# Kernel tuning notes

Measured on AMD Instinct MI355X. Metric: run time of the kernel, lower is better.

Reference implementation:

```python
import jax, jax.numpy as jnp
import numpy as np


def _segment_sparsemax(x, batch, B):
    """Per-group sparsemax over a flat ragged tensor.

    x: [N] float values; batch: [N] sorted int group ids in [0, B).
    Groups are contiguous, so an in-group descending sort is a stable
    lexsort on (batch, -x); per-group cumsum is a global cumsum minus the
    cumsum value just before each group's start offset.
    """
    N = x.shape[0]
    num_nodes = jax.ops.segment_sum(jnp.ones(N, jnp.int32), batch, num_segments=B)  # [B]
    start = jnp.concatenate([jnp.zeros(1, jnp.int32), jnp.cumsum(num_nodes)[:-1]])  # [B]

    # shift by per-group max for numerical stability (as in torch forward)
    gmax = jax.ops.segment_max(x, batch, num_segments=B)
    xs = x - gmax[batch]

    # descending sort within each contiguous group
    order = jnp.lexsort((-xs, batch))
    sx = xs[order]  # [N], group-wise descending; group layout unchanged

    # per-group cumulative sum via global cumsum + start offsets
    cs = jnp.cumsum(sx)
    off = jnp.where(start > 0, cs[jnp.maximum(start - 1, 0)], jnp.zeros((), sx.dtype))  # [B]
    seg_cs = cs - off[batch] - 1.0  # input_cumsum - 1.0

    # rho = 1..n_g within each group
    rho = (jnp.arange(N, dtype=jnp.int32) - start[batch] + 1).astype(xs.dtype)

    support = rho * sx > seg_cs  # [N] bool
    supp_size = jax.ops.segment_sum(support.astype(jnp.int32), batch, num_segments=B)  # [B]

    idx = jnp.maximum(supp_size + start - 1, 0)  # [B]
    tau = seg_cs[idx] / supp_size.astype(xs.dtype)  # [B]

    return jnp.maximum(xs - tau[batch], 0.0)


def setup_inputs() -> dict:
    key = jax.random.key(0)
    k1, k2 = jax.random.split(key)
    N = 8_388_608
    B = 4096
    x = jax.random.normal(k1, (N,), dtype=jnp.float32)
    batch = jnp.sort(jax.random.randint(k2, (N,), 0, B)).astype(jnp.int64)
    return {"x": x, "batch": batch, "num_groups": B}


def reference(x, batch, num_groups):
    batch = batch.astype(jnp.int32)
    return _segment_sparsemax(x, batch, int(num_groups))
```

## Files before the change

kernel.cpp:

```cpp
#include <hip/hip_runtime.h>

#define BLK 256
#define QPT 3
#define CAPB (QPT * BLK * 4)
#define CCAP 320


__device__ __forceinline__ float wave_max(float v) {
#pragma unroll
  for (int o = 32; o; o >>= 1) v = fmaxf(v, __shfl_xor(v, o));
  return v;
}
__device__ __forceinline__ float wave_sum(float v) {
#pragma unroll
  for (int o = 32; o; o >>= 1) v += __shfl_xor(v, o);
  return v;
}
__device__ __forceinline__ int wave_sum_i(int v) {
#pragma unroll
  for (int o = 32; o; o >>= 1) v += __shfl_xor(v, o);
  return v;
}

__device__ __forceinline__ void block_sum_cnt(float& s, int& c, float* redf, int* redi, int tid) {
  s = wave_sum(s); c = wave_sum_i(c);
  __syncthreads();
  if ((tid & 63) == 0) { redf[tid >> 6] = s; redi[tid >> 6] = c; }
  __syncthreads();
  s = redf[0] + redf[1] + redf[2] + redf[3];
  c = redi[0] + redi[1] + redi[2] + redi[3];
}


extern "C" __global__ void __launch_bounds__(256)
build_starts(const int* __restrict__ batch, int* __restrict__ starts,
             const int* __restrict__ pB, int N) {
  const int B = *pB;
  const long long tid = (long long)blockIdx.x * 256 + threadIdx.x;
  const long long i0 = tid * 8;
  if (i0 >= N) return;
  int v[8];
  if (i0 + 8 <= N) {
    const int4 a = *(const int4*)(batch + i0);
    const int4 b = *(const int4*)(batch + i0 + 4);
    v[0] = a.x; v[1] = a.y; v[2] = a.z; v[3] = a.w;
    v[4] = b.x; v[5] = b.y; v[6] = b.z; v[7] = b.w;
  } else {
#pragma unroll
    for (int t = 0; t < 8; ++t) v[t] = (i0 + t < N) ? batch[i0 + t] : 0;
  }
  int prev = (i0 == 0) ? -1 : batch[i0 - 1];
#pragma unroll
  for (int t = 0; t < 8; ++t) {
    if (i0 + t >= N) break;
    const int cur = v[t];
    for (int g = prev + 1; g <= cur; ++g) starts[g] = (int)(i0 + t);
    prev = cur;
  }
  if (i0 + 8 >= N) {
    for (int g = prev + 1; g <= B; ++g) starts[g] = N;
  }
}


extern "C" __global__ void __launch_bounds__(BLK)
sparsemax_groups(const float* __restrict__ x, const int* __restrict__ starts,
                 const int* __restrict__ pB, float* __restrict__ out, int N) {
  __shared__ float redf[4];
  __shared__ int   redi[4];
  __shared__ float cand[CCAP];
  __shared__ float sorted[64];
  __shared__ int   s_cnt;
  __shared__ float s_csum;
  __shared__ float s_tau;
  const int tid  = threadIdx.x;
  const int lane = tid & 63;
  const int w    = tid >> 6;
  const int B = *pB;

  for (int g = blockIdx.x; g < B; g += gridDim.x) {
    const int s = starts[g];
    const int e = starts[g + 1];
    const int n = e - s;
    if (n <= 0) continue;
    const int a0 = s & ~3;

    if (e - a0 <= CAPB) {
      float4 r[QPT];
      float lmax = -INFINITY;
#pragma unroll
      for (int j = 0; j < QPT; ++j) {
        const int idx = a0 + (j * BLK + tid) * 4;
        float4 v = make_float4(-INFINITY, -INFINITY, -INFINITY, -INFINITY);
        if (idx < e) {
          if (idx + 4 <= N) {
            v = *(const float4*)(x + idx);
          } else {
            if (idx + 0 < N) v.x = x[idx + 0];
            if (idx + 1 < N) v.y = x[idx + 1];
            if (idx + 2 < N) v.z = x[idx + 2];
            if (idx + 3 < N) v.w = x[idx + 3];
          }
          if (idx + 0 < s || idx + 0 >= e) v.x = -INFINITY;
          if (idx + 1 < s || idx + 1 >= e) v.y = -INFINITY;
          if (idx + 2 < s || idx + 2 >= e) v.z = -INFINITY;
          if (idx + 3 < s || idx + 3 >= e) v.w = -INFINITY;
        }
        r[j] = v;
        lmax = fmaxf(lmax, fmaxf(fmaxf(v.x, v.y), fmaxf(v.z, v.w)));
      }
      lmax = wave_max(lmax);
      if (lane == 0) redf[w] = lmax;
      if (tid == 0) { s_cnt = 0; s_csum = 0.0f; }
      __syncthreads();
      const float gmax = fmaxf(fmaxf(redf[0], redf[1]), fmaxf(redf[2], redf[3]));
      const float thr = gmax - 1.0f;

      float wsum = 0.0f;
#pragma unroll
      for (int j = 0; j < QPT; ++j) {
        const float vv[4] = {r[j].x, r[j].y, r[j].z, r[j].w};
#pragma unroll
        for (int t = 0; t < 4; ++t) {
          const bool p = vv[t] > thr;
          const unsigned long long bal = __ballot(p);
          if (bal) {
            int base = 0;
            if (lane == 0) base = atomicAdd(&s_cnt, __popcll(bal));
            base = __shfl(base, 0);
            if (p) {
              const int off = base + __popcll(bal & ((1ull << lane) - 1ull));
              if (off < CCAP) cand[off] = vv[t];
              wsum += vv[t] - gmax;
            }
          }
        }
      }
      wsum = wave_sum(wsum);
      if (lane == 0) atomicAdd(&s_csum, wsum);
      __syncthreads();
      const int c = s_cnt;

      if (c <= 64) {
        if (w == 0) {
          const float v = (lane < c) ? cand[lane] - gmax : 0.0f;
          int rank = 0;
          for (int q = 0; q < c; ++q) {
            const float t = cand[q] - gmax;
            rank += (t > v) || (t == v && q < lane);
          }
          if (lane < c) sorted[rank] = v;
          const float sv = (lane < c) ? sorted[lane] : 0.0f;
          float cs = sv;
#pragma unroll
          for (int o = 1; o < 64; o <<= 1) {
            const float t2 = __shfl_up(cs, o);
            if (lane >= o) cs += t2;
          }
          const int flag = (lane < c) && (sv * (float)(lane + 1) > cs - 1.0f);
          const unsigned long long bal2 = __ballot(flag);
          const int k = 63 - __clzll(bal2);
          const float csk = __shfl(cs, k);
          if (lane == 0) s_tau = (csk - 1.0f) / (float)(k + 1);
        }
      } else if (c <= CCAP) {
        if (w == 0) {
          float tau = (s_csum - 1.0f) / (float)c;
          int cnt = c;
          for (int it = 0; it < 64; ++it) {
            float s2 = 0.0f; int c2 = 0;
            for (int q = lane; q < c; q += 64) {
              const float vs = cand[q] - gmax;
              if (vs > tau) { s2 += vs; c2++; }
            }
            s2 = wave_sum(s2); c2 = wave_sum_i(c2);
            if (c2 == cnt || c2 == 0) break;
            tau = (s2 - 1.0f) / (float)c2; cnt = c2;
          }
          if (lane == 0) s_tau = tau;
        }
      } else {
        float tau = (s_csum - 1.0f) / (float)c;
        int cnt = c;
        for (int it = 0; it < 64; ++it) {
          float s2 = 0.0f; int c2 = 0;
#pragma unroll
          for (int j = 0; j < QPT; ++j) {
            const float vv[4] = {r[j].x, r[j].y, r[j].z, r[j].w};
#pragma unroll
            for (int t = 0; t < 4; ++t) {
              const float vs = vv[t] - gmax;
              if (vs > tau) { s2 += vs; c2++; }
            }
          }
          block_sum_cnt(s2, c2, redf, redi, tid);
          if (c2 == cnt || c2 == 0) break;
          tau = (s2 - 1.0f) / (float)c2; cnt = c2;
        }
        if (tid == 0) s_tau = tau;
      }
      __syncthreads();
      const float sub = s_tau + gmax;

#pragma unroll
      for (int j = 0; j < QPT; ++j) {
        const int idx = a0 + (j * BLK + tid) * 4;
        if (idx >= e) continue;
        if (idx >= s && idx + 4 <= e) {
          float4 o4;
          o4.x = fmaxf(r[j].x - sub, 0.0f);
          o4.y = fmaxf(r[j].y - sub, 0.0f);
          o4.z = fmaxf(r[j].z - sub, 0.0f);
          o4.w = fmaxf(r[j].w - sub, 0.0f);
          *(float4*)(out + idx) = o4;
        } else {
          const float vv[4] = {r[j].x, r[j].y, r[j].z, r[j].w};
#pragma unroll
          for (int t = 0; t < 4; ++t) {
            const int p2 = idx + t;
            if (p2 >= s && p2 < e) out[p2] = fmaxf(vv[t] - sub, 0.0f);
          }
        }
      }
    } else {
      float gmax = -INFINITY;
      for (int i = s + tid; i < e; i += BLK) gmax = fmaxf(gmax, x[i]);
      gmax = wave_max(gmax);
      if (lane == 0) redf[w] = gmax;
      __syncthreads();
      gmax = fmaxf(fmaxf(redf[0], redf[1]), fmaxf(redf[2], redf[3]));
      float bs = 0.0f; int bc = 0;
      for (int i = s + tid; i < e; i += BLK) {
        const float vs = x[i] - gmax;
        if (vs > -1.0f) { bs += vs; bc++; }
      }
      block_sum_cnt(bs, bc, redf, redi, tid);
      float tau = (bs - 1.0f) / (float)bc;
      int cntS = bc;
      for (int it = 0; it < 64; ++it) {
        float s2 = 0.0f; int c2 = 0;
        for (int i = s + tid; i < e; i += BLK) {
          const float vs = x[i] - gmax;
          if (vs > tau) { s2 += vs; c2++; }
        }
        block_sum_cnt(s2, c2, redf, redi, tid);
        if (c2 == cntS || c2 == 0) break;
        tau = (s2 - 1.0f) / (float)c2; cntS = c2;
      }
      const float sub = tau + gmax;
      for (int i = s + tid; i < e; i += BLK) out[i] = fmaxf(x[i] - sub, 0.0f);
    }
  }
}

extern "C" void kernel_launch(void* const* d_in, const int* in_sizes, int n_in,
                              void* d_out, int out_size, void* d_ws, size_t ws_size,
                              hipStream_t stream) {
  const float* x     = (const float*)d_in[0];
  const int*   batch = (const int*)d_in[1];
  const int*   pB    = (const int*)d_in[2];
  float*       out   = (float*)d_out;
  const int N = in_sizes[0];

  int* starts = (int*)d_ws;

  const int g1 = (N + 2047) / 2048;
  build_starts<<<dim3(g1), dim3(256), 0, stream>>>(batch, starts, pB, N);
  sparsemax_groups<<<dim3(4096), dim3(BLK), 0, stream>>>(x, starts, pB, out, N);
}
```

Before: 111.9 us.

## Fuse group boundary search into sparsemax kernel via wave-parallel lower bound

Removes the separate build_starts pass, which read the whole batch array and wrote a starts table, and the extra kernel launch. Each block now finds its own group start and end with a 65-way wave-parallel search over the sorted batch array, using two wavefronts concurrently. This trades a full streaming read of batch for a few rounds of dependent, latency-bound scattered loads per group, plus extra barriers in the group loop.

```diff
diff --git a/kernel.cpp b/kernel.cpp
--- a/kernel.cpp
+++ b/kernel.cpp
@@ -31,45 +31,32 @@
   c = redi[0] + redi[1] + redi[2] + redi[3];
 }
 
-
-extern "C" __global__ void __launch_bounds__(256)
-build_starts(const int* __restrict__ batch, int* __restrict__ starts,
-             const int* __restrict__ pB, int N) {
-  const int B = *pB;
-  const long long tid = (long long)blockIdx.x * 256 + threadIdx.x;
-  const long long i0 = tid * 8;
-  if (i0 >= N) return;
-  int v[8];
-  if (i0 + 8 <= N) {
-    const int4 a = *(const int4*)(batch + i0);
-    const int4 b = *(const int4*)(batch + i0 + 4);
-    v[0] = a.x; v[1] = a.y; v[2] = a.z; v[3] = a.w;
-    v[4] = b.x; v[5] = b.y; v[6] = b.z; v[7] = b.w;
-  } else {
-#pragma unroll
-    for (int t = 0; t < 8; ++t) v[t] = (i0 + t < N) ? batch[i0 + t] : 0;
+__device__ __forceinline__ int wave_lower_bound(const int* __restrict__ batch, int N,
+                                                int target, int lane) {
+  int lo = 0, hi = N;
+  while (hi > lo) {
+    const long long span = hi - lo;
+    const int m = lo + (int)((span * (long long)(lane + 1)) / 65);
+    const int flag = (batch[m] < target) ? 1 : 0;
+    const unsigned long long bal = __ballot(flag);
+    const int c = __popcll(bal);
+    int nlo = lo, nhi = hi;
+    if (c > 0)  nlo = lo + (int)((span * (long long)c) / 65) + 1;
+    if (c < 64) nhi = lo + (int)((span * (long long)(c + 1)) / 65);
+    lo = nlo; hi = nhi;
   }
-  int prev = (i0 == 0) ? -1 : batch[i0 - 1];
-#pragma unroll
-  for (int t = 0; t < 8; ++t) {
-    if (i0 + t >= N) break;
-    const int cur = v[t];
-    for (int g = prev + 1; g <= cur; ++g) starts[g] = (int)(i0 + t);
-    prev = cur;
-  }
-  if (i0 + 8 >= N) {
-    for (int g = prev + 1; g <= B; ++g) starts[g] = N;
-  }
+  return lo;
 }
 
 
 extern "C" __global__ void __launch_bounds__(BLK)
-sparsemax_groups(const float* __restrict__ x, const int* __restrict__ starts,
-                 const int* __restrict__ pB, float* __restrict__ out, int N) {
+sparsemax_fused(const float* __restrict__ x, const int* __restrict__ batch,
+                const int* __restrict__ pB, float* __restrict__ out, int N) {
   __shared__ float redf[4];
   __shared__ int   redi[4];
   __shared__ float cand[CCAP];
   __shared__ float sorted[64];
+  __shared__ int   s_se[2];
   __shared__ int   s_cnt;
   __shared__ float s_csum;
   __shared__ float s_tau;
@@ -79,10 +66,18 @@
   const int B = *pB;
 
   for (int g = blockIdx.x; g < B; g += gridDim.x) {
-    const int s = starts[g];
-    const int e = starts[g + 1];
+    if (w == 0) {
+      const int v = wave_lower_bound(batch, N, g, lane);
+      if (lane == 0) { s_se[0] = v; s_cnt = 0; s_csum = 0.0f; }
+    } else if (w == 1) {
+      const int v = wave_lower_bound(batch, N, g + 1, lane);
+      if (lane == 0) s_se[1] = v;
+    }
+    __syncthreads();
+    const int s = s_se[0];
+    const int e = s_se[1];
     const int n = e - s;
-    if (n <= 0) continue;
+    if (n <= 0) { __syncthreads(); continue; }
     const int a0 = s & ~3;
 
     if (e - a0 <= CAPB) {
@@ -111,7 +106,6 @@
       }
       lmax = wave_max(lmax);
       if (lane == 0) redf[w] = lmax;
-      if (tid == 0) { s_cnt = 0; s_csum = 0.0f; }
       __syncthreads();
       const float gmax = fmaxf(fmaxf(redf[0], redf[1]), fmaxf(redf[2], redf[3]));
       const float thr = gmax - 1.0f;
@@ -250,6 +244,7 @@
       const float sub = tau + gmax;
       for (int i = s + tid; i < e; i += BLK) out[i] = fmaxf(x[i] - sub, 0.0f);
     }
+    __syncthreads();
   }
 }
 
@@ -262,9 +257,5 @@
   float*       out   = (float*)d_out;
   const int N = in_sizes[0];
 
-  int* starts = (int*)d_ws;
-
-  const int g1 = (N + 2047) / 2048;
-  build_starts<<<dim3(g1), dim3(256), 0, stream>>>(batch, starts, pB, N);
-  sparsemax_groups<<<dim3(4096), dim3(BLK), 0, stream>>>(x, starts, pB, out, N);
-}
+  sparsemax_fused<<<dim3(4096), dim3(BLK), 0, stream>>>(x, batch, pB, out, N);
+}
```

Measured after the change: 116.0 us. +3.6%, slower.
